# Kernel optimization log

Measured on AMD Instinct MI355X. Metric: run time of the kernel, lower is better.

The kernel has to match this reference:

```python
import jax, jax.numpy as jnp
import numpy as np

TOPK = 8
BN_EPS = 1e-5


def setup_inputs() -> dict:
    key = jax.random.key(0)
    ks = jax.random.split(key, 5)
    b, n, d = 2, 1024, 1024
    h, nk, kd = 8, 256, 128  # num_heads, num_keys (sqrt(65536)), key_dims
    ne = nk * nk             # 65536 experts
    scale = 0.02
    return {
        "inputs": jax.random.normal(ks[0], (b, n, d), jnp.float32),
        "gamma": jnp.ones((d,), jnp.float32),
        "beta": jnp.zeros((d,), jnp.float32),
        "w_q": jax.random.normal(ks[1], (2 * h * kd, d), jnp.float32) * scale,
        "keys": jax.random.normal(ks[2], (h, nk, 2, kd), jnp.float32) * scale,
        "key_in": jax.random.normal(ks[3], (ne, d), jnp.float32) * scale,
        "key_out": jax.random.normal(ks[4], (ne, d), jnp.float32) * scale,
    }


def reference(inputs, gamma, beta, w_q, keys, key_in, key_out):
    b, n, d = inputs.shape
    h, nk, _, kd = keys.shape
    k = TOPK

    # BatchNorm1d over flattened tokens (training-mode batch statistics)
    x = inputs.reshape(b * n, d)
    mu = jnp.mean(x, axis=0)
    var = jnp.mean(jnp.square(x - mu), axis=0)  # biased var, as torch BN
    xn = (x - mu) * jax.lax.rsqrt(var + BN_EPS) * gamma + beta

    # query projection -> (2, b, n, h, kd)
    q = (xn @ w_q.T).reshape(b, n, 2, h, kd).transpose(2, 0, 1, 3, 4)

    # similarity with product keys: (2, b, n, h, nk)
    sim = jnp.einsum("pbnhd,hkpd->pbnhk", q, keys)

    # stage 1: per-half top-k
    s, i = jax.lax.top_k(sim, k)          # (2, b, n, h, k)
    sx, sy = s[0], s[1]
    ix, iy = i[0], i[1]

    # stage 2: cartesian combine then top-k of k*k
    all_scores = (sx[..., :, None] + sy[..., None, :]).reshape(b, n, h, k * k)
    all_idx = (ix[..., :, None] * nk + iy[..., None, :]).reshape(b, n, h, k * k)
    scores, pk = jax.lax.top_k(all_scores, k)          # (b, n, h, k)
    idx = jnp.take_along_axis(all_idx, pk, axis=-1)    # (b, n, h, k)

    # gather expert vectors: (b, n, h, k, d)
    w_down = key_in[idx]
    w_up = key_out[idx]

    o = jnp.einsum("bnd,bnhkd->bnhk", inputs, w_down)
    o = jax.nn.gelu(o, approximate=False) * jax.nn.softmax(scores, axis=-1)
    return jnp.einsum("bnhk,bnhkd->bnd", o, w_up)
```

## Files before the change

### kernel.cpp

```cpp
#include <hip/hip_runtime.h>
#include <math.h>

#define TT 2048
#define DD 1024
#define HH 8
#define NKK 256
#define KDD 128
#define TK 8
#define NEE 65536

#define WS_PS    0
#define WS_PQ    262144
#define WS_A     524288
#define WS_B2    528384
#define WS_XN    1048576
#define WS_Q     9437184
#define WS_SIM   26214400
#define WS_IDX   59768832
#define WS_SMW   60293120

__global__ __launch_bounds__(256) void bn_partial(const float* __restrict__ x,
    double* __restrict__ ps, double* __restrict__ pq)
{
    int col = blockIdx.x * 256 + threadIdx.x;
    int r0 = blockIdx.y * 64;
    double s = 0.0, q = 0.0;
    for (int r = 0; r < 64; ++r) {
        double v = (double)x[(size_t)(r0 + r) * DD + col];
        s += v; q += v * v;
    }
    ps[(size_t)blockIdx.y * DD + col] = s;
    pq[(size_t)blockIdx.y * DD + col] = q;
}

__global__ __launch_bounds__(256) void bn_final(const double* __restrict__ ps,
    const double* __restrict__ pq, const float* __restrict__ gamma,
    const float* __restrict__ beta, float* __restrict__ Aout, float* __restrict__ Bout)
{
    int col = blockIdx.x * 256 + threadIdx.x;
    double s = 0.0, q = 0.0;
    for (int g = 0; g < 32; ++g) { s += ps[(size_t)g * DD + col]; q += pq[(size_t)g * DD + col]; }
    double mu = s / 2048.0;
    double var = q / 2048.0 - mu * mu;
    double rstd = 1.0 / sqrt(var + 1e-5);
    Aout[col] = (float)((double)gamma[col] * rstd);
    Bout[col] = (float)((double)beta[col] - mu * (double)gamma[col] * rstd);
}

__global__ __launch_bounds__(256) void xn_kernel(const float* __restrict__ x,
    const float* __restrict__ A, const float* __restrict__ B2, float* __restrict__ XN)
{
    int i = blockIdx.x * 256 + threadIdx.x;
    float4 v = ((const float4*)x)[i];
    int c = (i & 255) << 2;
    v.x = v.x * A[c + 0] + B2[c + 0];
    v.y = v.y * A[c + 1] + B2[c + 1];
    v.z = v.z * A[c + 2] + B2[c + 2];
    v.w = v.w * A[c + 3] + B2[c + 3];
    ((float4*)XN)[i] = v;
}

__global__ __launch_bounds__(256) void gemm_nt(
    const float* __restrict__ Abase, const float* __restrict__ Bbase,
    float* __restrict__ Cbase, int lda, int ldb, int ldc, int Kdim, int mode)
{
    const float* A = Abase; const float* B = Bbase; float* C = Cbase;
    if (mode == 1) {
        int z = blockIdx.z;
        int p = z >> 3, h = z & 7;
        A += (size_t)z * 128;
        B += (size_t)h * (NKK * 2 * KDD) + (size_t)p * KDD;
        C += (size_t)p * ((size_t)TT * HH * NKK) + (size_t)h * NKK;
    }
    __shared__ float As[16][132];
    __shared__ float Bs[16][132];
    int tid = threadIdx.x;
    int tx = tid & 15, ty = tid >> 4;
    int m0 = blockIdx.x * 128, n0 = blockIdx.y * 128;
    float acc[8][8];
#pragma unroll
    for (int i = 0; i < 8; ++i)
#pragma unroll
        for (int j = 0; j < 8; ++j) acc[i][j] = 0.f;

    for (int k0 = 0; k0 < Kdim; k0 += 16) {
#pragma unroll
        for (int it = 0; it < 2; ++it) {
            int li = tid + it * 256;
            int row = li >> 2;
            int kc = (li & 3) << 2;
            float4 va = *(const float4*)(A + (size_t)(m0 + row) * lda + k0 + kc);
            As[kc + 0][row] = va.x; As[kc + 1][row] = va.y;
            As[kc + 2][row] = va.z; As[kc + 3][row] = va.w;
            float4 vb = *(const float4*)(B + (size_t)(n0 + row) * ldb + k0 + kc);
            Bs[kc + 0][row] = vb.x; Bs[kc + 1][row] = vb.y;
            Bs[kc + 2][row] = vb.z; Bs[kc + 3][row] = vb.w;
        }
        __syncthreads();
#pragma unroll
        for (int k = 0; k < 16; ++k) {
            float a[8], b[8];
            *(float4*)&a[0] = *(const float4*)&As[k][ty * 4];
            *(float4*)&a[4] = *(const float4*)&As[k][64 + ty * 4];
            *(float4*)&b[0] = *(const float4*)&Bs[k][tx * 4];
            *(float4*)&b[4] = *(const float4*)&Bs[k][64 + tx * 4];
#pragma unroll
            for (int i = 0; i < 8; ++i)
#pragma unroll
                for (int j = 0; j < 8; ++j) acc[i][j] += a[i] * b[j];
        }
        __syncthreads();
    }
#pragma unroll
    for (int i = 0; i < 8; ++i) {
        int m = m0 + ((i < 4) ? (ty * 4 + i) : (64 + ty * 4 + (i - 4)));
        float4 c0 = make_float4(acc[i][0], acc[i][1], acc[i][2], acc[i][3]);
        float4 c1 = make_float4(acc[i][4], acc[i][5], acc[i][6], acc[i][7]);
        *(float4*)(C + (size_t)m * ldc + n0 + tx * 4) = c0;
        *(float4*)(C + (size_t)m * ldc + n0 + 64 + tx * 4) = c1;
    }
}

__global__ __launch_bounds__(256) void topk_kernel(
    const float* __restrict__ SIM, int* __restrict__ IDX, float* __restrict__ SMW)
{
    int gw = blockIdx.x * 4 + (threadIdx.x >> 6);
    int lane = threadIdx.x & 63;
    int t = gw >> 3, h = gw & 7;

    float vx = 0.f, vy = 0.f; int vix = 0, viy = 0;

    {
        const float* s = SIM + ((size_t)t * HH + h) * NKK;
        float v0 = s[lane], v1 = s[lane + 64], v2 = s[lane + 128], v3 = s[lane + 192];
#pragma unroll
        for (int it = 0; it < 8; ++it) {
            float bv = v0; int bj = 0;
            if (v1 > bv) { bv = v1; bj = 1; }
            if (v2 > bv) { bv = v2; bj = 2; }
            if (v3 > bv) { bv = v3; bj = 3; }
            int mi = lane + (bj << 6);
            float mv = bv;
#pragma unroll
            for (int off = 1; off < 64; off <<= 1) {
                float ov = __shfl_xor(mv, off);
                int oi = __shfl_xor(mi, off);
                if (ov > mv || (ov == mv && oi < mi)) { mv = ov; mi = oi; }
            }
            if ((lane >> 3) == it) { vx = mv; vix = mi; }
            if (mi == lane)            v0 = -INFINITY;
            else if (mi == lane + 64)  v1 = -INFINITY;
            else if (mi == lane + 128) v2 = -INFINITY;
            else if (mi == lane + 192) v3 = -INFINITY;
        }
    }
    {
        const float* s = SIM + (size_t)TT * HH * NKK + ((size_t)t * HH + h) * NKK;
        float v0 = s[lane], v1 = s[lane + 64], v2 = s[lane + 128], v3 = s[lane + 192];
#pragma unroll
        for (int it = 0; it < 8; ++it) {
            float bv = v0; int bj = 0;
            if (v1 > bv) { bv = v1; bj = 1; }
            if (v2 > bv) { bv = v2; bj = 2; }
            if (v3 > bv) { bv = v3; bj = 3; }
            int mi = lane + (bj << 6);
            float mv = bv;
#pragma unroll
            for (int off = 1; off < 64; off <<= 1) {
                float ov = __shfl_xor(mv, off);
                int oi = __shfl_xor(mi, off);
                if (ov > mv || (ov == mv && oi < mi)) { mv = ov; mi = oi; }
            }
            if ((lane & 7) == it) { vy = mv; viy = mi; }
            if (mi == lane)            v0 = -INFINITY;
            else if (mi == lane + 64)  v1 = -INFINITY;
            else if (mi == lane + 128) v2 = -INFINITY;
            else if (mi == lane + 192) v3 = -INFINITY;
        }
    }

    float mycs = vx + vy;
    int cidx = vix * NKK + viy;
    float s2[8]; int wi2[8];
#pragma unroll
    for (int it = 0; it < 8; ++it) {
        float mv = mycs; int ml = lane;
#pragma unroll
        for (int off = 1; off < 64; off <<= 1) {
            float ov = __shfl_xor(mv, off);
            int ol = __shfl_xor(ml, off);
            if (ov > mv || (ov == mv && ol < ml)) { mv = ov; ml = ol; }
        }
        s2[it] = mv;
        wi2[it] = __shfl(cidx, ml);
        if (lane == ml) mycs = -INFINITY;
    }
    float e[8]; float esum = 0.f;
#pragma unroll
    for (int it = 0; it < 8; ++it) { e[it] = expf(s2[it] - s2[0]); esum += e[it]; }
    float inv = 1.f / esum;
    if (lane == 0) {
        int base = (t * HH + h) * TK;
#pragma unroll
        for (int it = 0; it < 8; ++it) { IDX[base + it] = wi2[it]; SMW[base + it] = e[it] * inv; }
    }
}

__global__ __launch_bounds__(256) void expert_kernel(
    const float* __restrict__ x, const int* __restrict__ IDX,
    const float* __restrict__ SMW, const float* __restrict__ key_in,
    const float* __restrict__ key_out, float* __restrict__ out)
{
    int t = blockIdx.x;
    int tid = threadIdx.x, lane = tid & 63, w = tid >> 6;
    __shared__ float xs[DD];
    __shared__ float part[4][DD];
    *(float4*)&xs[tid * 4] = *(const float4*)(x + (size_t)t * DD + tid * 4);
    __syncthreads();
    float4 xin[4];
#pragma unroll
    for (int r = 0; r < 4; ++r) xin[r] = *(const float4*)&xs[r * 256 + lane * 4];
    float4 acc[4];
#pragma unroll
    for (int r = 0; r < 4; ++r) acc[r] = make_float4(0.f, 0.f, 0.f, 0.f);

    for (int hh2 = 0; hh2 < 2; ++hh2) {
        int hh = w * 2 + hh2;
        for (int k = 0; k < TK; ++k) {
            int base = (t * HH + hh) * TK + k;
            int e = IDX[base];
            float wt = SMW[base];
            const float* ki = key_in + (size_t)e * DD;
            const float* ko = key_out + (size_t)e * DD;
            float4 kin[4], kout[4];
#pragma unroll
            for (int r = 0; r < 4; ++r) kin[r] = *(const float4*)(ki + r * 256 + lane * 4);
#pragma unroll
            for (int r = 0; r < 4; ++r) kout[r] = *(const float4*)(ko + r * 256 + lane * 4);
            float p = 0.f;
#pragma unroll
            for (int r = 0; r < 4; ++r)
                p += xin[r].x * kin[r].x + xin[r].y * kin[r].y
                   + xin[r].z * kin[r].z + xin[r].w * kin[r].w;
#pragma unroll
            for (int off = 1; off < 64; off <<= 1) p += __shfl_xor(p, off);
            float g = 0.5f * p * (1.f + erff(p * 0.70710678118654752440f));
            float go = g * wt;
#pragma unroll
            for (int r = 0; r < 4; ++r) {
                acc[r].x += go * kout[r].x; acc[r].y += go * kout[r].y;
                acc[r].z += go * kout[r].z; acc[r].w += go * kout[r].w;
            }
        }
    }
#pragma unroll
    for (int r = 0; r < 4; ++r) *(float4*)&part[w][r * 256 + lane * 4] = acc[r];
    __syncthreads();
    int c = tid * 4;
    float4 s0 = *(const float4*)&part[0][c];
    float4 s1 = *(const float4*)&part[1][c];
    float4 s2 = *(const float4*)&part[2][c];
    float4 s3 = *(const float4*)&part[3][c];
    float4 o;
    o.x = (s0.x + s1.x) + (s2.x + s3.x);
    o.y = (s0.y + s1.y) + (s2.y + s3.y);
    o.z = (s0.z + s1.z) + (s2.z + s3.z);
    o.w = (s0.w + s1.w) + (s2.w + s3.w);
    *(float4*)(out + (size_t)t * DD + c) = o;
}

extern "C" void kernel_launch(void* const* d_in, const int* in_sizes, int n_in,
                              void* d_out, int out_size, void* d_ws, size_t ws_size,
                              hipStream_t stream)
{
    const float* x       = (const float*)d_in[0];
    const float* gamma   = (const float*)d_in[1];
    const float* beta    = (const float*)d_in[2];
    const float* w_q     = (const float*)d_in[3];
    const float* keys    = (const float*)d_in[4];
    const float* key_in  = (const float*)d_in[5];
    const float* key_out = (const float*)d_in[6];
    float* out = (float*)d_out;
    char* ws = (char*)d_ws;

    double* ps  = (double*)(ws + WS_PS);
    double* pq  = (double*)(ws + WS_PQ);
    float*  Aw  = (float*)(ws + WS_A);
    float*  B2w = (float*)(ws + WS_B2);
    float*  XN  = (float*)(ws + WS_XN);
    float*  Q   = (float*)(ws + WS_Q);
    float*  SIMw= (float*)(ws + WS_SIM);
    int*    IDXw= (int*)(ws + WS_IDX);
    float*  SMWw= (float*)(ws + WS_SMW);

    bn_partial<<<dim3(4, 32), 256, 0, stream>>>(x, ps, pq);
    bn_final<<<4, 256, 0, stream>>>(ps, pq, gamma, beta, Aw, B2w);
    xn_kernel<<<2048, 256, 0, stream>>>(x, Aw, B2w, XN);
    gemm_nt<<<dim3(16, 16, 1), 256, 0, stream>>>(XN, w_q, Q, 1024, 1024, 2048, 1024, 0);
    gemm_nt<<<dim3(16, 2, 16), 256, 0, stream>>>(Q, keys, SIMw, 2048, 256, 2048, 128, 1);
    topk_kernel<<<4096, 256, 0, stream>>>(SIMw, IDXw, SMWw);
    expert_kernel<<<2048, 256, 0, stream>>>(x, IDXw, SMWw, key_in, key_out, out);
}
```

Measured before the change: 381.3 us.

## Split expert kernel into separate logits and weighted-combine kernels

Splits the fused per-token expert kernel in two. One kernel computes the GELU-times-softmax weight for each (token, head, k) over 16384 blocks, and a second gathers the 64 key_out rows per token and accumulates them with float4 loads. The goal is more parallelism and less register pressure than one block per token holding both key_in and key_out vectors, and it also removes the shared-memory partial reduction. The cost is an extra launch, a small intermediate buffer written over the SIM workspace, and reloading x for each of the 8 head blocks per token.

```diff
diff --git a/kernel.cpp b/kernel.cpp
--- a/kernel.cpp
+++ b/kernel.cpp
@@ -16,6 +16,7 @@
 #define WS_XN    1048576
 #define WS_Q     9437184
 #define WS_SIM   26214400
+#define WS_GO    26214400
 #define WS_IDX   59768832
 #define WS_SMW   60293120
 
@@ -206,67 +207,66 @@
     }
 }
 
-__global__ __launch_bounds__(256) void expert_kernel(
+__global__ __launch_bounds__(256) void logits_kernel(
     const float* __restrict__ x, const int* __restrict__ IDX,
     const float* __restrict__ SMW, const float* __restrict__ key_in,
-    const float* __restrict__ key_out, float* __restrict__ out)
-{
-    int t = blockIdx.x;
+    float* __restrict__ GO)
+{
+    int th = blockIdx.x;
+    int t = th >> 3;
     int tid = threadIdx.x, lane = tid & 63, w = tid >> 6;
     __shared__ float xs[DD];
-    __shared__ float part[4][DD];
     *(float4*)&xs[tid * 4] = *(const float4*)(x + (size_t)t * DD + tid * 4);
     __syncthreads();
     float4 xin[4];
 #pragma unroll
     for (int r = 0; r < 4; ++r) xin[r] = *(const float4*)&xs[r * 256 + lane * 4];
-    float4 acc[4];
-#pragma unroll
-    for (int r = 0; r < 4; ++r) acc[r] = make_float4(0.f, 0.f, 0.f, 0.f);
-
-    for (int hh2 = 0; hh2 < 2; ++hh2) {
-        int hh = w * 2 + hh2;
-        for (int k = 0; k < TK; ++k) {
-            int base = (t * HH + hh) * TK + k;
-            int e = IDX[base];
-            float wt = SMW[base];
-            const float* ki = key_in + (size_t)e * DD;
-            const float* ko = key_out + (size_t)e * DD;
-            float4 kin[4], kout[4];
-#pragma unroll
-            for (int r = 0; r < 4; ++r) kin[r] = *(const float4*)(ki + r * 256 + lane * 4);
-#pragma unroll
-            for (int r = 0; r < 4; ++r) kout[r] = *(const float4*)(ko + r * 256 + lane * 4);
-            float p = 0.f;
-#pragma unroll
-            for (int r = 0; r < 4; ++r)
-                p += xin[r].x * kin[r].x + xin[r].y * kin[r].y
-                   + xin[r].z * kin[r].z + xin[r].w * kin[r].w;
-#pragma unroll
-            for (int off = 1; off < 64; off <<= 1) p += __shfl_xor(p, off);
+
+#pragma unroll
+    for (int kk = 0; kk < 2; ++kk) {
+        int base = th * TK + w * 2 + kk;
+        int e = IDX[base];
+        const float* ki = key_in + (size_t)e * DD;
+        float4 kin[4];
+#pragma unroll
+        for (int r = 0; r < 4; ++r) kin[r] = *(const float4*)(ki + r * 256 + lane * 4);
+        float p = 0.f;
+#pragma unroll
+        for (int r = 0; r < 4; ++r)
+            p += xin[r].x * kin[r].x + xin[r].y * kin[r].y
+               + xin[r].z * kin[r].z + xin[r].w * kin[r].w;
+#pragma unroll
+        for (int off = 1; off < 64; off <<= 1) p += __shfl_xor(p, off);
+        if (lane == 0) {
             float g = 0.5f * p * (1.f + erff(p * 0.70710678118654752440f));
-            float go = g * wt;
-#pragma unroll
-            for (int r = 0; r < 4; ++r) {
-                acc[r].x += go * kout[r].x; acc[r].y += go * kout[r].y;
-                acc[r].z += go * kout[r].z; acc[r].w += go * kout[r].w;
-            }
-        }
-    }
-#pragma unroll
-    for (int r = 0; r < 4; ++r) *(float4*)&part[w][r * 256 + lane * 4] = acc[r];
+            GO[base] = g * SMW[base];
+        }
+    }
+}
+
+__global__ __launch_bounds__(256) void combine_kernel(
+    const float* __restrict__ GO, const int* __restrict__ IDX,
+    const float* __restrict__ key_out, float* __restrict__ out)
+{
+    int t = blockIdx.x;
+    int tid = threadIdx.x;
+    __shared__ int es[64];
+    __shared__ float wsh[64];
+    if (tid < 64) {
+        es[tid] = IDX[t * 64 + tid];
+        wsh[tid] = GO[t * 64 + tid];
+    }
     __syncthreads();
     int c = tid * 4;
-    float4 s0 = *(const float4*)&part[0][c];
-    float4 s1 = *(const float4*)&part[1][c];
-    float4 s2 = *(const float4*)&part[2][c];
-    float4 s3 = *(const float4*)&part[3][c];
-    float4 o;
-    o.x = (s0.x + s1.x) + (s2.x + s3.x);
-    o.y = (s0.y + s1.y) + (s2.y + s3.y);
-    o.z = (s0.z + s1.z) + (s2.z + s3.z);
-    o.w = (s0.w + s1.w) + (s2.w + s3.w);
-    *(float4*)(out + (size_t)t * DD + c) = o;
+    float4 acc = make_float4(0.f, 0.f, 0.f, 0.f);
+#pragma unroll 8
+    for (int j = 0; j < 64; ++j) {
+        const float4 v = *(const float4*)(key_out + (size_t)es[j] * DD + c);
+        float wj = wsh[j];
+        acc.x += wj * v.x; acc.y += wj * v.y;
+        acc.z += wj * v.z; acc.w += wj * v.w;
+    }
+    *(float4*)(out + (size_t)t * DD + c) = acc;
 }
 
 extern "C" void kernel_launch(void* const* d_in, const int* in_sizes, int n_in,
@@ -292,6 +292,7 @@
     float*  SIMw= (float*)(ws + WS_SIM);
     int*    IDXw= (int*)(ws + WS_IDX);
     float*  SMWw= (float*)(ws + WS_SMW);
+    float*  GOw = (float*)(ws + WS_GO);
 
     bn_partial<<<dim3(4, 32), 256, 0, stream>>>(x, ps, pq);
     bn_final<<<4, 256, 0, stream>>>(ps, pq, gamma, beta, Aw, B2w);
@@ -299,5 +300,6 @@
     gemm_nt<<<dim3(16, 16, 1), 256, 0, stream>>>(XN, w_q, Q, 1024, 1024, 2048, 1024, 0);
     gemm_nt<<<dim3(16, 2, 16), 256, 0, stream>>>(Q, keys, SIMw, 2048, 256, 2048, 128, 1);
     topk_kernel<<<4096, 256, 0, stream>>>(SIMw, IDXw, SMWw);
-    expert_kernel<<<2048, 256, 0, stream>>>(x, IDXw, SMWw, key_in, key_out, out);
-}
+    logits_kernel<<<16384, 256, 0, stream>>>(x, IDXw, SMWw, key_in, GOw);
+    combine_kernel<<<2048, 256, 0, stream>>>(GOw, IDXw, key_out, out);
+}
```

After: 395.3 us. 3.7% more time.

## Use split-bf16 MFMA for query GEMM with fp32 fixup for near-tie top-k

Applied to the files above, without the earlier changes.

The fp32 SIMT query projection GEMM is replaced by an MFMA kernel. Each operand is split into high and low bf16 halves, and three products are accumulated to approximate fp32 precision. Because the small error could flip top-k selections, the top-k kernel now computes the 9th-ranked value and flags rows whose selection margins fall below a threshold. A fixup kernel then recomputes those rows' queries and similarities in exact fp32. This adds conversion kernels for w_q and XN and a 16384-block fixup launch in exchange for much faster matrix math.

```diff
diff --git a/kernel.cpp b/kernel.cpp
--- a/kernel.cpp
+++ b/kernel.cpp
@@ -9,15 +9,24 @@
 #define TK 8
 #define NEE 65536
 
+#define DELTA 2e-5f
+
 #define WS_PS    0
 #define WS_PQ    262144
 #define WS_A     524288
 #define WS_B2    528384
-#define WS_XN    1048576
+#define WS_FLAG  532480
+#define WS_XNH   1048576
+#define WS_XNL   5242880
 #define WS_Q     9437184
 #define WS_SIM   26214400
+#define WS_WQH   26214400
+#define WS_WQL   30408704
 #define WS_IDX   59768832
 #define WS_SMW   60293120
+
+typedef short bf16x8 __attribute__((ext_vector_type(8)));
+typedef float f32x4 __attribute__((ext_vector_type(4)));
 
 __global__ __launch_bounds__(256) void bn_partial(const float* __restrict__ x,
     double* __restrict__ ps, double* __restrict__ pq)
@@ -47,8 +56,18 @@
     Bout[col] = (float)((double)beta[col] - mu * (double)gamma[col] * rstd);
 }
 
+__device__ __forceinline__ void split_bf16(float v, unsigned short& h, unsigned short& l)
+{
+    __bf16 hb = (__bf16)v;
+    float hf = (float)hb;
+    __bf16 lb = (__bf16)(v - hf);
+    h = __builtin_bit_cast(unsigned short, hb);
+    l = __builtin_bit_cast(unsigned short, lb);
+}
+
 __global__ __launch_bounds__(256) void xn_kernel(const float* __restrict__ x,
-    const float* __restrict__ A, const float* __restrict__ B2, float* __restrict__ XN)
+    const float* __restrict__ A, const float* __restrict__ B2,
+    unsigned short* __restrict__ XNh, unsigned short* __restrict__ XNl)
 {
     int i = blockIdx.x * 256 + threadIdx.x;
     float4 v = ((const float4*)x)[i];
@@ -57,7 +76,102 @@
     v.y = v.y * A[c + 1] + B2[c + 1];
     v.z = v.z * A[c + 2] + B2[c + 2];
     v.w = v.w * A[c + 3] + B2[c + 3];
-    ((float4*)XN)[i] = v;
+    ushort4 h, l;
+    split_bf16(v.x, h.x, l.x); split_bf16(v.y, h.y, l.y);
+    split_bf16(v.z, h.z, l.z); split_bf16(v.w, h.w, l.w);
+    ((ushort4*)XNh)[i] = h;
+    ((ushort4*)XNl)[i] = l;
+}
+
+__global__ __launch_bounds__(256) void wq_convert(const float* __restrict__ wq,
+    unsigned short* __restrict__ Wh, unsigned short* __restrict__ Wl)
+{
+    int i = blockIdx.x * 256 + threadIdx.x;
+    float4 v = ((const float4*)wq)[i];
+    ushort4 h, l;
+    split_bf16(v.x, h.x, l.x); split_bf16(v.y, h.y, l.y);
+    split_bf16(v.z, h.z, l.z); split_bf16(v.w, h.w, l.w);
+    ((ushort4*)Wh)[i] = h;
+    ((ushort4*)Wl)[i] = l;
+}
+
+#define LSTR 40
+__global__ __launch_bounds__(256) void gemm_q_mfma(
+    const unsigned short* __restrict__ Ah, const unsigned short* __restrict__ Al,
+    const unsigned short* __restrict__ Bh, const unsigned short* __restrict__ Bl,
+    float* __restrict__ C)
+{
+    __shared__ unsigned short sAh[128 * LSTR], sAl[128 * LSTR];
+    __shared__ unsigned short sBh[128 * LSTR], sBl[128 * LSTR];
+    int tid = threadIdx.x;
+    int lane = tid & 63, w = tid >> 6;
+    int wm = w >> 1, wn = w & 1;
+    int m0 = blockIdx.x * 128, n0 = blockIdx.y * 128;
+
+    f32x4 acc[4][4];
+#pragma unroll
+    for (int i = 0; i < 4; ++i)
+#pragma unroll
+        for (int j = 0; j < 4; ++j)
+#pragma unroll
+            for (int r = 0; r < 4; ++r) acc[i][j][r] = 0.f;
+
+    int srow = tid >> 1;
+    int kc0 = (tid & 1) << 1;
+    size_t gA = ((size_t)(m0 + srow) << 10) + (kc0 << 3);
+    size_t gB = ((size_t)(n0 + srow) << 10) + (kc0 << 3);
+    int ls = srow * LSTR + (kc0 << 3);
+
+    int ao[4], bo[4];
+#pragma unroll
+    for (int i = 0; i < 4; ++i) {
+        ao[i] = (wm * 64 + i * 16 + (lane & 15)) * LSTR + ((lane >> 4) << 3);
+        bo[i] = (wn * 64 + i * 16 + (lane & 15)) * LSTR + ((lane >> 4) << 3);
+    }
+
+    for (int k0 = 0; k0 < 1024; k0 += 32) {
+        float4 vah0 = *(const float4*)(Ah + gA + k0);
+        float4 vah1 = *(const float4*)(Ah + gA + k0 + 8);
+        float4 val0 = *(const float4*)(Al + gA + k0);
+        float4 val1 = *(const float4*)(Al + gA + k0 + 8);
+        float4 vbh0 = *(const float4*)(Bh + gB + k0);
+        float4 vbh1 = *(const float4*)(Bh + gB + k0 + 8);
+        float4 vbl0 = *(const float4*)(Bl + gB + k0);
+        float4 vbl1 = *(const float4*)(Bl + gB + k0 + 8);
+        *(float4*)(sAh + ls) = vah0;  *(float4*)(sAh + ls + 8) = vah1;
+        *(float4*)(sAl + ls) = val0;  *(float4*)(sAl + ls + 8) = val1;
+        *(float4*)(sBh + ls) = vbh0;  *(float4*)(sBh + ls + 8) = vbh1;
+        *(float4*)(sBl + ls) = vbl0;  *(float4*)(sBl + ls + 8) = vbl1;
+        __syncthreads();
+
+        bf16x8 fah[4], fal[4], fbh[4], fbl[4];
+#pragma unroll
+        for (int i = 0; i < 4; ++i) {
+            fah[i] = *(const bf16x8*)(sAh + ao[i]);
+            fal[i] = *(const bf16x8*)(sAl + ao[i]);
+            fbh[i] = *(const bf16x8*)(sBh + bo[i]);
+            fbl[i] = *(const bf16x8*)(sBl + bo[i]);
+        }
+#pragma unroll
+        for (int i = 0; i < 4; ++i)
+#pragma unroll
+            for (int j = 0; j < 4; ++j) {
+                acc[i][j] = __builtin_amdgcn_mfma_f32_16x16x32_bf16(fah[i], fbh[j], acc[i][j], 0, 0, 0);
+                acc[i][j] = __builtin_amdgcn_mfma_f32_16x16x32_bf16(fah[i], fbl[j], acc[i][j], 0, 0, 0);
+                acc[i][j] = __builtin_amdgcn_mfma_f32_16x16x32_bf16(fal[i], fbh[j], acc[i][j], 0, 0, 0);
+            }
+        __syncthreads();
+    }
+
+    int crow = m0 + wm * 64 + ((lane >> 4) << 2);
+    int ccol = n0 + wn * 64 + (lane & 15);
+#pragma unroll
+    for (int i = 0; i < 4; ++i)
+#pragma unroll
+        for (int j = 0; j < 4; ++j)
+#pragma unroll
+            for (int r = 0; r < 4; ++r)
+                C[(size_t)(crow + i * 16 + r) * 2048 + ccol + j * 16] = acc[i][j][r];
 }
 
 __global__ __launch_bounds__(256) void gemm_nt(
@@ -121,69 +235,42 @@
     }
 }
 
-__global__ __launch_bounds__(256) void topk_kernel(
-    const float* __restrict__ SIM, int* __restrict__ IDX, float* __restrict__ SMW)
-{
-    int gw = blockIdx.x * 4 + (threadIdx.x >> 6);
-    int lane = threadIdx.x & 63;
-    int t = gw >> 3, h = gw & 7;
-
-    float vx = 0.f, vy = 0.f; int vix = 0, viy = 0;
-
-    {
-        const float* s = SIM + ((size_t)t * HH + h) * NKK;
-        float v0 = s[lane], v1 = s[lane + 64], v2 = s[lane + 128], v3 = s[lane + 192];
-#pragma unroll
-        for (int it = 0; it < 8; ++it) {
-            float bv = v0; int bj = 0;
-            if (v1 > bv) { bv = v1; bj = 1; }
-            if (v2 > bv) { bv = v2; bj = 2; }
-            if (v3 > bv) { bv = v3; bj = 3; }
-            int mi = lane + (bj << 6);
-            float mv = bv;
-#pragma unroll
-            for (int off = 1; off < 64; off <<= 1) {
-                float ov = __shfl_xor(mv, off);
-                int oi = __shfl_xor(mi, off);
-                if (ov > mv || (ov == mv && oi < mi)) { mv = ov; mi = oi; }
-            }
-            if ((lane >> 3) == it) { vx = mv; vix = mi; }
-            if (mi == lane)            v0 = -INFINITY;
-            else if (mi == lane + 64)  v1 = -INFINITY;
-            else if (mi == lane + 128) v2 = -INFINITY;
-            else if (mi == lane + 192) v3 = -INFINITY;
-        }
-    }
-    {
-        const float* s = SIM + (size_t)TT * HH * NKK + ((size_t)t * HH + h) * NKK;
-        float v0 = s[lane], v1 = s[lane + 64], v2 = s[lane + 128], v3 = s[lane + 192];
-#pragma unroll
-        for (int it = 0; it < 8; ++it) {
-            float bv = v0; int bj = 0;
-            if (v1 > bv) { bv = v1; bj = 1; }
-            if (v2 > bv) { bv = v2; bj = 2; }
-            if (v3 > bv) { bv = v3; bj = 3; }
-            int mi = lane + (bj << 6);
-            float mv = bv;
-#pragma unroll
-            for (int off = 1; off < 64; off <<= 1) {
-                float ov = __shfl_xor(mv, off);
-                int oi = __shfl_xor(mi, off);
-                if (ov > mv || (ov == mv && oi < mi)) { mv = ov; mi = oi; }
-            }
-            if ((lane & 7) == it) { vy = mv; viy = mi; }
-            if (mi == lane)            v0 = -INFINITY;
-            else if (mi == lane + 64)  v1 = -INFINITY;
-            else if (mi == lane + 128) v2 = -INFINITY;
-            else if (mi == lane + 192) v3 = -INFINITY;
-        }
-    }
-
+__device__ __forceinline__ void stage1_half(float v0, float v1, float v2, float v3,
+    int lane, int mode, float& keep_v, int& keep_i, float& g7, float& g8)
+{
+#pragma unroll
+    for (int it = 0; it < 9; ++it) {
+        float bv = v0; int bj = 0;
+        if (v1 > bv) { bv = v1; bj = 1; }
+        if (v2 > bv) { bv = v2; bj = 2; }
+        if (v3 > bv) { bv = v3; bj = 3; }
+        int mi = lane + (bj << 6);
+        float mv = bv;
+#pragma unroll
+        for (int off = 1; off < 64; off <<= 1) {
+            float ov = __shfl_xor(mv, off);
+            int oi = __shfl_xor(mi, off);
+            if (ov > mv || (ov == mv && oi < mi)) { mv = ov; mi = oi; }
+        }
+        int keeper = (mode == 0) ? (lane >> 3) : (lane & 7);
+        if (it < 8 && keeper == it) { keep_v = mv; keep_i = mi; }
+        if (it == 7) g7 = mv;
+        if (it == 8) g8 = mv;
+        if (mi == lane)            v0 = -INFINITY;
+        else if (mi == lane + 64)  v1 = -INFINITY;
+        else if (mi == lane + 128) v2 = -INFINITY;
+        else if (mi == lane + 192) v3 = -INFINITY;
+    }
+}
+
+__device__ __forceinline__ float stage2_write(float vx, float vy, int vix, int viy,
+    int lane, int base, int* __restrict__ IDX, float* __restrict__ SMW)
+{
     float mycs = vx + vy;
     int cidx = vix * NKK + viy;
-    float s2[8]; int wi2[8];
-#pragma unroll
-    for (int it = 0; it < 8; ++it) {
+    float s2[9]; int wi2[8];
+#pragma unroll
+    for (int it = 0; it < 9; ++it) {
         float mv = mycs; int ml = lane;
 #pragma unroll
         for (int off = 1; off < 64; off <<= 1) {
@@ -192,7 +279,7 @@
             if (ov > mv || (ov == mv && ol < ml)) { mv = ov; ml = ol; }
         }
         s2[it] = mv;
-        wi2[it] = __shfl(cidx, ml);
+        if (it < 8) wi2[it] = __shfl(cidx, ml);
         if (lane == ml) mycs = -INFINITY;
     }
     float e[8]; float esum = 0.f;
@@ -200,10 +287,93 @@
     for (int it = 0; it < 8; ++it) { e[it] = expf(s2[it] - s2[0]); esum += e[it]; }
     float inv = 1.f / esum;
     if (lane == 0) {
-        int base = (t * HH + h) * TK;
 #pragma unroll
         for (int it = 0; it < 8; ++it) { IDX[base + it] = wi2[it]; SMW[base + it] = e[it] * inv; }
     }
+    return s2[7] - s2[8];
+}
+
+__global__ __launch_bounds__(256) void topk_kernel(
+    const float* __restrict__ SIM, int* __restrict__ IDX, float* __restrict__ SMW,
+    int* __restrict__ FLAG)
+{
+    int gw = blockIdx.x * 4 + (threadIdx.x >> 6);
+    int lane = threadIdx.x & 63;
+    int t = gw >> 3, h = gw & 7;
+
+    float vx = 0.f, vy = 0.f; int vix = 0, viy = 0;
+    float g7a, g8a, g7b, g8b;
+
+    const float* s0 = SIM + ((size_t)t * HH + h) * NKK;
+    stage1_half(s0[lane], s0[lane + 64], s0[lane + 128], s0[lane + 192],
+                lane, 0, vx, vix, g7a, g8a);
+    const float* s1 = SIM + (size_t)TT * HH * NKK + ((size_t)t * HH + h) * NKK;
+    stage1_half(s1[lane], s1[lane + 64], s1[lane + 128], s1[lane + 192],
+                lane, 1, vy, viy, g7b, g8b);
+
+    float gap2 = stage2_write(vx, vy, vix, viy, lane, gw * TK, IDX, SMW);
+    if (lane == 0) {
+        FLAG[gw] = ((g7a - g8a) < DELTA) | ((g7b - g8b) < DELTA) | (gap2 < DELTA);
+    }
+}
+
+__global__ __launch_bounds__(64) void fixup_kernel(
+    const float* __restrict__ x, const float* __restrict__ Aw,
+    const float* __restrict__ B2w, const float* __restrict__ w_q,
+    const float* __restrict__ keys, const int* __restrict__ FLAG,
+    int* __restrict__ IDX, float* __restrict__ SMW)
+{
+    int row = blockIdx.x;
+    if (!FLAG[row]) return;
+    int t = row >> 3, h = row & 7;
+    int lane = threadIdx.x;
+    __shared__ float xs[DD];
+    __shared__ float qs[2][KDD];
+    __shared__ float sims[2][NKK];
+
+    for (int c = lane * 4; c < DD; c += 256) {
+        float4 v = *(const float4*)(x + (size_t)t * DD + c);
+        v.x = v.x * Aw[c + 0] + B2w[c + 0];
+        v.y = v.y * Aw[c + 1] + B2w[c + 1];
+        v.z = v.z * Aw[c + 2] + B2w[c + 2];
+        v.w = v.w * Aw[c + 3] + B2w[c + 3];
+        *(float4*)&xs[c] = v;
+    }
+    __syncthreads();
+
+    for (int p = 0; p < 2; ++p)
+        for (int j = 0; j < 2; ++j) {
+            int kd = lane + j * 64;
+            const float* wr = w_q + ((size_t)((p * HH + h) * KDD) + kd) * DD;
+            float acc = 0.f;
+            for (int d = 0; d < DD; d += 4) {
+                float4 wv = *(const float4*)(wr + d);
+                acc += xs[d] * wv.x + xs[d + 1] * wv.y + xs[d + 2] * wv.z + xs[d + 3] * wv.w;
+            }
+            qs[p][kd] = acc;
+        }
+    __syncthreads();
+
+    for (int p = 0; p < 2; ++p)
+        for (int j = 0; j < 4; ++j) {
+            int key = lane + j * 64;
+            const float* kr = keys + (((size_t)h * NKK + key) * 2 + p) * KDD;
+            float acc = 0.f;
+            for (int d = 0; d < KDD; d += 4) {
+                float4 kv = *(const float4*)(kr + d);
+                acc += qs[p][d] * kv.x + qs[p][d + 1] * kv.y + qs[p][d + 2] * kv.z + qs[p][d + 3] * kv.w;
+            }
+            sims[p][key] = acc;
+        }
+    __syncthreads();
+
+    float vx = 0.f, vy = 0.f; int vix = 0, viy = 0;
+    float d0, d1, d2, d3;
+    stage1_half(sims[0][lane], sims[0][lane + 64], sims[0][lane + 128], sims[0][lane + 192],
+                lane, 0, vx, vix, d0, d1);
+    stage1_half(sims[1][lane], sims[1][lane + 64], sims[1][lane + 128], sims[1][lane + 192],
+                lane, 1, vy, viy, d2, d3);
+    stage2_write(vx, vy, vix, viy, lane, row * TK, IDX, SMW);
 }
 
 __global__ __launch_bounds__(256) void expert_kernel(
@@ -287,7 +457,11 @@
     double* pq  = (double*)(ws + WS_PQ);
     float*  Aw  = (float*)(ws + WS_A);
     float*  B2w = (float*)(ws + WS_B2);
-    float*  XN  = (float*)(ws + WS_XN);
+    int*    FLAGw = (int*)(ws + WS_FLAG);
+    unsigned short* XNh = (unsigned short*)(ws + WS_XNH);
+    unsigned short* XNl = (unsigned short*)(ws + WS_XNL);
+    unsigned short* WQh = (unsigned short*)(ws + WS_WQH);
+    unsigned short* WQl = (unsigned short*)(ws + WS_WQL);
     float*  Q   = (float*)(ws + WS_Q);
     float*  SIMw= (float*)(ws + WS_SIM);
     int*    IDXw= (int*)(ws + WS_IDX);
@@ -295,9 +469,11 @@
 
     bn_partial<<<dim3(4, 32), 256, 0, stream>>>(x, ps, pq);
     bn_final<<<4, 256, 0, stream>>>(ps, pq, gamma, beta, Aw, B2w);
-    xn_kernel<<<2048, 256, 0, stream>>>(x, Aw, B2w, XN);
-    gemm_nt<<<dim3(16, 16, 1), 256, 0, stream>>>(XN, w_q, Q, 1024, 1024, 2048, 1024, 0);
+    xn_kernel<<<2048, 256, 0, stream>>>(x, Aw, B2w, XNh, XNl);
+    wq_convert<<<2048, 256, 0, stream>>>(w_q, WQh, WQl);
+    gemm_q_mfma<<<dim3(16, 16), 256, 0, stream>>>(XNh, XNl, WQh, WQl, Q);
     gemm_nt<<<dim3(16, 2, 16), 256, 0, stream>>>(Q, keys, SIMw, 2048, 256, 2048, 128, 1);
-    topk_kernel<<<4096, 256, 0, stream>>>(SIMw, IDXw, SMWw);
+    topk_kernel<<<4096, 256, 0, stream>>>(SIMw, IDXw, SMWw, FLAGw);
+    fixup_kernel<<<16384, 64, 0, stream>>>(x, Aw, B2w, w_q, keys, FLAGw, IDXw, SMWw);
     expert_kernel<<<2048, 256, 0, stream>>>(x, IDXw, SMWw, key_in, key_out, out);
 }
```

After: 443.6 us. 16.3% more time.
